# Kernel tuning notes

Hardware: AMD Instinct MI355X
Metric: run time of the kernel (lower is better)

Reference implementation:

```python
import jax, jax.numpy as jnp
import numpy as np


def _conv3x3(x, w):
    # x: [B,C,H,W], w: [O,I,3,3], SAME padding, no bias
    return jax.lax.conv_general_dilated(x, w, (1, 1), 'SAME',
                                        dimension_numbers=('NCHW', 'OIHW', 'NCHW'))


def _instance_norm(x, g, b, eps=1e-6):
    # normalize over spatial dims per (batch, channel)
    m = x.mean(axis=(2, 3), keepdims=True)
    v = x.var(axis=(2, 3), keepdims=True)
    xn = (x - m) * jax.lax.rsqrt(v + eps)
    return xn * g[None, :, None, None] + b[None, :, None, None]


def setup_inputs() -> dict:
    key = jax.random.key(0)
    ks = jax.random.split(key, 16)
    B, N, L = 1, 128, 256
    d_msa, d_pair, d_h = 256, 128, 32
    f32 = jnp.float32
    inp = {
        'msa': jax.random.normal(ks[0], (B, N, L, d_msa), f32),
        'pair': jax.random.normal(ks[1], (B, L, L, d_pair), f32),
        # LayerNorm(d_msa)
        'ln_g': jnp.ones((d_msa,), f32),
        'ln_b': jnp.zeros((d_msa,), f32),
        # proj_left / proj_right (lecun-normal-ish scale, zero bias)
        'Wl': jax.random.normal(ks[2], (d_msa, d_h), f32) * (1.0 / np.sqrt(d_msa)),
        'bl': jnp.zeros((d_h,), f32),
        'Wr': jax.random.normal(ks[3], (d_msa, d_h), f32) * (1.0 / np.sqrt(d_msa)),
        'br': jnp.zeros((d_h,), f32),
        # proj_out: (d_h*d_h) -> d_pair
        'Wo': jax.random.normal(ks[4], (d_h * d_h, d_pair), f32) * (1.0 / np.sqrt(d_h * d_h)),
        'bo': jnp.zeros((d_pair,), f32),
        # proj_down: (2*d_pair) -> d_pair, torch init eye_ -> identity block
        'Wd': jnp.concatenate([jnp.eye(d_pair, dtype=f32),
                               jnp.zeros((d_pair, d_pair), f32)], axis=0),
        'bd': jnp.zeros((d_pair,), f32),
        # ResBlock2D: two 3x3 convs (no bias) + affine InstanceNorm each
        'conv1': jax.random.normal(ks[5], (d_pair, d_pair, 3, 3), f32) * (1.0 / np.sqrt(9 * d_pair)),
        'in1_g': jnp.ones((d_pair,), f32),
        'in1_b': jnp.zeros((d_pair,), f32),
        'conv2': jax.random.normal(ks[6], (d_pair, d_pair, 3, 3), f32) * (1.0 / np.sqrt(9 * d_pair)),
        'in2_g': jnp.ones((d_pair,), f32),
        'in2_b': jnp.zeros((d_pair,), f32),
    }
    return inp


def reference(msa, pair, ln_g, ln_b, Wl, bl, Wr, br, Wo, bo, Wd, bd,
              conv1, in1_g, in1_b, conv2, in2_g, in2_b):
    B, N, L, _ = msa.shape
    # LayerNorm over d_msa (eps=1e-5, torch default)
    mu = msa.mean(-1, keepdims=True)
    var = msa.var(-1, keepdims=True)
    msa_n = (msa - mu) * jax.lax.rsqrt(var + 1e-5) * ln_g + ln_b
    left = msa_n @ Wl + bl                      # [B,N,L,h]
    right = (msa_n @ Wr + br) / float(N)        # [B,N,L,h]
    # MSA outer product over sequences: [B,L,L,h,h] -> [B,L,L,h*h]
    op = jnp.einsum('bsli,bsmj->blmij', left, right).reshape(B, L, L, -1)
    out = op @ Wo + bo                          # [B,L,L,d_pair]
    p = jnp.concatenate([pair, out], axis=-1) @ Wd + bd  # proj_down
    # ResidualNetwork(1 block): NCHW
    x = p.transpose(0, 3, 1, 2)
    h = _conv3x3(x, conv1)
    h = jax.nn.elu(_instance_norm(h, in1_g, in1_b))
    # dropout is identity at inference
    h = _conv3x3(h, conv2)
    h = _instance_norm(h, in2_g, in2_b)
    x = jax.nn.elu(x + h)
    return x.transpose(0, 2, 3, 1)              # [B,L,L,d_pair]
```

## Files before the change

### kernel.cpp

```cpp
#include <hip/hip_runtime.h>
#include <math.h>

#define LL 256
#define NS 128
#define DM 256
#define DH 32
#define DP 128
#define HW 65536

using u16 = unsigned short;
typedef __attribute__((ext_vector_type(8))) short s8v;
typedef __attribute__((ext_vector_type(4))) short s4v;
typedef __attribute__((ext_vector_type(4))) float f4v;

#define MFMA(a, b, c) __builtin_amdgcn_mfma_f32_16x16x32_bf16((a), (b), (c), 0, 0, 0)

__device__ __forceinline__ u16 f2bf(float f) {
  unsigned u = __float_as_uint(f);
  u = (u + 0x7FFFu + ((u >> 16) & 1u)) >> 16;
  return (u16)u;
}
__device__ __forceinline__ unsigned cvtpk2(float lo, float hi) {
  unsigned r;
  asm("v_cvt_pk_bf16_f32 %0, %1, %2" : "=v"(r) : "v"(lo), "v"(hi));
  return r;
}
__device__ __forceinline__ float bf2f(u16 h) { return __uint_as_float(((unsigned)h) << 16); }
__device__ __forceinline__ float elu1(float v) { return v > 0.f ? v : expm1f(v); }
__device__ __forceinline__ s8v zero8() {
  s8v v;
  #pragma unroll
  for (int j = 0; j < 8; ++j) v[j] = 0;
  return v;
}


__device__ __forceinline__ void prep_convw(const float* __restrict__ w,
                                           u16* __restrict__ wP, int idx)
{
  int h = idx & 3, co = (idx >> 2) & 127, kk = (idx >> 9) & 3, tap = idx >> 11;
  s8v o;
  #pragma unroll
  for (int j = 0; j < 8; ++j) {
    int ci = kk * 32 + h * 8 + j;
    o[j] = (short)f2bf(w[((size_t)co * DP + ci) * 9 + tap]);
  }
  *(s8v*)(wP + (size_t)idx * 8) = o;
}

__global__ __launch_bounds__(256) void k_prep_ln(
    const float* __restrict__ Wl, const float* __restrict__ Wr,
    const float* __restrict__ Wo, const float* __restrict__ Wd,
    const float* __restrict__ conv1, const float* __restrict__ conv2,
    const float* __restrict__ pair,
    const float* __restrict__ msa, const float* __restrict__ ln_g,
    const float* __restrict__ ln_b,
    u16* __restrict__ WlrF, u16* __restrict__ WoF, u16* __restrict__ WdF,
    u16* __restrict__ wP1, u16* __restrict__ wP2, u16* __restrict__ pairF,
    u16* __restrict__ msaF)
{
  __shared__ alignas(16) u16 buf[16 * 264];
  int bx = blockIdx.x, t = threadIdx.x;
  if (bx < 64) {
    int o = bx * 256 + t;
    int tile = o >> 6, u = o & 63;
    int cblk = tile >> 5, j = tile & 31;
    int kslot = u >> 4, cl = u & 15;
    int c = cblk * 16 + cl;
    s8v v;
    #pragma unroll
    for (int e = 0; e < 8; ++e) {
      int i = kslot * 8 + e;
      v[e] = (short)f2bf(Wo[(size_t)(i * 32 + j) * DP + c]);
    }
    *(s8v*)(WoF + (size_t)o * 8) = v;
  } else if (bx < 80) {
    int o = (bx - 64) * 256 + t;
    int tile = o >> 6, u = o & 63;
    int cblk = tile >> 3, kch = tile & 7;
    int kslot = u >> 4, cl = u & 15;
    int c = cblk * 16 + cl;
    s8v v;
    #pragma unroll
    for (int e = 0; e < 8; ++e) {
      int k = kch * 32 + kslot * 8 + e;
      v[e] = (short)f2bf(Wd[(size_t)k * DP + c]);
    }
    *(s8v*)(WdF + (size_t)o * 8) = v;
  } else if (bx < 88) {
    int o = (bx - 80) * 256 + t;
    int tile = o >> 6, u = o & 63;
    int nblk = tile >> 3, kch = tile & 7;
    int kslot = u >> 4, cl = u & 15;
    int n = nblk * 16 + cl;
    s8v v;
    #pragma unroll
    for (int e = 0; e < 8; ++e) {
      int k = kch * 32 + kslot * 8 + e;
      float x = (n < 32) ? Wl[k * DH + n] : Wr[k * DH + (n - 32)];
      v[e] = (short)f2bf(x);
    }
    *(s8v*)(WlrF + (size_t)o * 8) = v;
  } else if (bx < 160) {
    prep_convw(conv1, wP1, (bx - 88) * 256 + t);
  } else if (bx < 232) {
    prep_convw(conv2, wP2, (bx - 160) * 256 + t);
  } else if (bx < 4328) {
    int pb = bx - 232;
    #pragma unroll
    for (int it = 0; it < 2; ++it) {
      int idx = it * 256 + t;
      int pix = idx >> 5, f4i = idx & 31;
      float4 v = ((const float4*)pair)[(size_t)(pb * 16 + pix) * 32 + f4i];
      s4v o;
      o[0] = (short)f2bf(v.x); o[1] = (short)f2bf(v.y);
      o[2] = (short)f2bf(v.z); o[3] = (short)f2bf(v.w);
      *(s4v*)(buf + pix * 136 + f4i * 4) = o;
    }
    __syncthreads();
    int kch = t >> 6, u = t & 63;
    int kslot = u >> 4, cl = u & 15;
    int k0 = kch * 32 + kslot * 8;
    s8v v = *(const s8v*)(buf + cl * 136 + k0);
    *(s8v*)(pairF + ((size_t)pb * 256 + t) * 8) = v;
  } else {
    int bid = bx - 4328;
    int lane = t & 63, wid = t >> 6;
    int row0 = bid * 16;
    const float4 gv = ((const float4*)ln_g)[lane];
    const float4 bv = ((const float4*)ln_b)[lane];
    #pragma unroll
    for (int rr = 0; rr < 4; ++rr) {
      int row = row0 + wid * 4 + rr;
      float4 v = ((const float4*)(msa + (size_t)row * DM))[lane];
      float s = v.x + v.y + v.z + v.w;
      float q = v.x * v.x + v.y * v.y + v.z * v.z + v.w * v.w;
      #pragma unroll
      for (int off = 32; off; off >>= 1) { s += __shfl_down(s, off); q += __shfl_down(q, off); }
      s = __shfl(s, 0); q = __shfl(q, 0);
      float mean = s * (1.f / DM);
      float var  = q * (1.f / DM) - mean * mean;
      float rstd = rsqrtf(var + 1e-5f);
      s4v o;
      o[0] = (short)f2bf((v.x - mean) * rstd * gv.x + bv.x);
      o[1] = (short)f2bf((v.y - mean) * rstd * gv.y + bv.y);
      o[2] = (short)f2bf((v.z - mean) * rstd * gv.z + bv.z);
      o[3] = (short)f2bf((v.w - mean) * rstd * gv.w + bv.w);
      *(s4v*)(buf + (wid * 4 + rr) * 264 + lane * 4) = o;
    }
    __syncthreads();
    #pragma unroll
    for (int it = 0; it < 2; ++it) {
      int o = it * 256 + t;
      int kch = o >> 6, kslot = (o >> 4) & 3, rr = o & 15;
      int k0 = kch * 32 + kslot * 8;
      s8v v = *(const s8v*)(buf + rr * 264 + k0);
      *(s8v*)(msaF + (size_t)bid * 4096 + (size_t)o * 8) = v;
    }
  }
}

__global__ __launch_bounds__(256) void k_gemm_lr(const u16* __restrict__ msaF,
                                                 const u16* __restrict__ WlrF,
                                                 const float* __restrict__ bl,
                                                 const float* __restrict__ br,
                                                 u16* __restrict__ leftT,
                                                 u16* __restrict__ rightT)
{
  int lane = threadIdx.x & 63, wid = threadIdx.x >> 6;
  int sIdx = blockIdx.x;
  f4v acc[4][4] = {};
  #pragma unroll
  for (int ks = 0; ks < 8; ++ks) {
    s8v a[4], bb[4];
    #pragma unroll
    for (int mi = 0; mi < 4; ++mi)
      a[mi] = *(const s8v*)(msaF + ((size_t)(sIdx * 16 + wid * 4 + mi) * 8 + ks) * 512 + lane * 8);
    #pragma unroll
    for (int ni = 0; ni < 4; ++ni)
      bb[ni] = *(const s8v*)(WlrF + ((size_t)(ni * 8 + ks)) * 512 + lane * 8);
    #pragma unroll
    for (int mi = 0; mi < 4; ++mi)
      #pragma unroll
      for (int ni = 0; ni < 4; ++ni)
        acc[mi][ni] = MFMA(a[mi], bb[ni], acc[mi][ni]);
  }
  #pragma unroll
  for (int mi = 0; mi < 4; ++mi) {
    #pragma unroll
    for (int ni = 0; ni < 4; ++ni) {
      int n = ni * 16 + (lane & 15);
      #pragma unroll
      for (int r = 0; r < 4; ++r) {
        int l = wid * 64 + mi * 16 + (lane >> 4) * 4 + r;
        float v = acc[mi][ni][r];
        if (n < 32) {
          leftT[((size_t)l * 32 + n) * 128 + sIdx] = f2bf(v + bl[n]);
        } else {
          rightT[((size_t)l * 32 + (n - 32)) * 128 + sIdx] =
              f2bf((v + br[n - 32]) * (1.f / NS));
        }
      }
    }
  }
}

__global__ __launch_bounds__(256) void k_fragpack(const u16* __restrict__ leftT,
                                                  const u16* __restrict__ rightT,
                                                  u16* __restrict__ leftF,
                                                  u16* __restrict__ rightF)
{
  __shared__ alignas(16) u16 lds[64 * 136];
  int t = threadIdx.x, bx = blockIdx.x;
  bool isR = bx >= 128;
  int blk = isR ? (bx - 128) : bx;
  #pragma unroll
  for (int it = 0; it < 4; ++it) {
    int u = it * 256 + t;
    int row = u >> 4, sc = u & 15;
    const u16* src;
    if (!isR) {
      src = leftT + ((size_t)(blk * 64 + row)) * 128 + sc * 8;
    } else {
      int gcol = blk * 64 + row;
      int mg = gcol >> 10, rem = gcol & 1023;
      int jc = rem >> 8, nc = rem & 255;
      int m = mg * 32 + (nc >> 3), j = jc * 8 + (nc & 7);
      src = rightT + ((size_t)(m * 32 + j)) * 128 + sc * 8;
    }
    *(s8v*)(lds + row * 136 + sc * 8) = *(const s8v*)src;
  }
  __syncthreads();
  u16* dst = (isR ? rightF : leftF) + (size_t)blk * 8192;
  #pragma unroll
  for (int it = 0; it < 4; ++it) {
    int o = it * 256 + t;
    int tloc = o >> 6, u = o & 63;
    int rb = tloc >> 2, sc2 = tloc & 3;
    int kslot = u >> 4, rr = u & 15;
    int row = rb * 16 + rr, s0 = sc2 * 32 + kslot * 8;
    *(s8v*)(dst + (size_t)o * 8) = *(const s8v*)(lds + row * 136 + s0);
  }
}

__global__ __launch_bounds__(512, 4) void k_fused(
    const u16* __restrict__ leftF, const u16* __restrict__ rightF,
    const u16* __restrict__ WoF, const u16* __restrict__ pairF,
    const u16* __restrict__ WdF, const float* __restrict__ bo,
    const float* __restrict__ bd, u16* __restrict__ pN)
{
  __shared__ alignas(16) u16 Als[8192];
  __shared__ alignas(16) u16 opL[16384];
  __shared__ alignas(16) u16 obL[8192];
  int t = threadIdx.x, lane = t & 63, w = t >> 6;
  int rlo = lane & 15, slot = lane >> 4;
  int b = blockIdx.x;
  int mg = b & 7, lp = b >> 3;
  int l0 = lp * 2, m0 = mg * 32;

  #pragma unroll
  for (int i = 0; i < 2; ++i) {
    int u = t + 512 * i;
    *(s8v*)(Als + (size_t)u * 8) = *(const s8v*)(leftF + (size_t)lp * 8192 + (size_t)u * 8);
  }

  f4v acc2[4] = {};
  s8v bb[8];
  #pragma unroll
  for (int ks = 0; ks < 4; ++ks)
    #pragma unroll
    for (int ni = 0; ni < 2; ++ni)
      bb[ks * 2 + ni] = *(const s8v*)(rightF +
          ((size_t)((mg * 64 + 0 * 16 + w * 2 + ni) * 4 + ks)) * 512 + lane * 8);
  __syncthreads();

  #pragma unroll
  for (int jc = 0; jc < 4; ++jc) {
    f4v acc1[4][2] = {};
    __builtin_amdgcn_s_setprio(1);
    #pragma unroll
    for (int ks = 0; ks < 4; ++ks) {
      s8v a[4];
      #pragma unroll
      for (int mi = 0; mi < 4; ++mi)
        a[mi] = *(const s8v*)(Als + (size_t)(mi * 4 + ks) * 512 + lane * 8);
      #pragma unroll
      for (int mi = 0; mi < 4; ++mi)
        #pragma unroll
        for (int ni = 0; ni < 2; ++ni)
          acc1[mi][ni] = MFMA(a[mi], bb[ks * 2 + ni], acc1[mi][ni]);
    }
    __builtin_amdgcn_s_setprio(0);
    #pragma unroll
    for (int mi = 0; mi < 4; ++mi) {
      int i0 = (mi & 1) * 16 + slot * 4;
      int lLoc = mi >> 1;
      int kslot = (i0 >> 3) & 3;
      #pragma unroll
      for (int ni = 0; ni < 2; ++ni) {
        int n = w * 32 + ni * 16 + rlo;
        int pix = lLoc * 32 + (n >> 3);
        int jj = n & 7;
        uint2 o2;
        o2.x = cvtpk2(acc1[mi][ni][0], acc1[mi][ni][1]);
        o2.y = cvtpk2(acc1[mi][ni][2], acc1[mi][ni][3]);
        int byte = ((pix >> 4) * 8 + jj) * 1024 +
                   (kslot * 16 + ((pix & 15) ^ jj)) * 16 + (i0 & 7) * 2;
        *(uint2*)((char*)opL + byte) = o2;
      }
    }
    s8v wb[8];
    #pragma unroll
    for (int ks = 0; ks < 8; ++ks)
      wb[ks] = *(const s8v*)(WoF + ((size_t)(w * 32 + jc * 8 + ks)) * 512 + lane * 8);
    __syncthreads();
    __builtin_amdgcn_s_setprio(1);
    #pragma unroll
    for (int ks = 0; ks < 8; ++ks) {
      s8v a[4];
      #pragma unroll
      for (int mi = 0; mi < 4; ++mi) {
        int byte = (mi * 8 + ks) * 1024 + (slot * 16 + (rlo ^ ks)) * 16;
        a[mi] = *(const s8v*)((const char*)opL + byte);
      }
      #pragma unroll
      for (int mi = 0; mi < 4; ++mi)
        acc2[mi] = MFMA(a[mi], wb[ks], acc2[mi]);
    }
    __builtin_amdgcn_s_setprio(0);
    if (jc < 3) {
      #pragma unroll
      for (int ks = 0; ks < 4; ++ks)
        #pragma unroll
        for (int ni = 0; ni < 2; ++ni)
          bb[ks * 2 + ni] = *(const s8v*)(rightF +
              ((size_t)((mg * 64 + (jc + 1) * 16 + w * 2 + ni) * 4 + ks)) * 512 + lane * 8);
    }
    __syncthreads();
  }

  {
    int c = w * 16 + rlo;
    float bias = bo[c];
    #pragma unroll
    for (int mi = 0; mi < 4; ++mi)
      #pragma unroll
      for (int r = 0; r < 4; ++r) {
        int pix = mi * 16 + slot * 4 + r;
        int byte = (pix * 256 + c * 2) ^ ((pix & 7) << 4);
        *(u16*)((char*)obL + byte) = f2bf(acc2[mi][r] + bias);
      }
  }
  __syncthreads();

  int wr = w >> 2, wcq = w & 3;
  int pix0 = wr * 32, c0 = wcq * 32;
  {
    f4v acc[2][2] = {};
    #pragma unroll
    for (int ks = 0; ks < 4; ++ks) {
      s8v a[2], b2[2];
      #pragma unroll
      for (int mi = 0; mi < 2; ++mi) {
        int pb = (l0 + wr) * 16 + (m0 >> 4) + mi;
        a[mi] = *(const s8v*)(pairF + ((size_t)(pb * 4 + ks)) * 512 + lane * 8);
      }
      #pragma unroll
      for (int ni = 0; ni < 2; ++ni) {
        int cblk = wcq * 2 + ni;
        b2[ni] = *(const s8v*)(WdF + ((size_t)(cblk * 8 + ks)) * 512 + lane * 8);
      }
      #pragma unroll
      for (int mi = 0; mi < 2; ++mi)
        #pragma unroll
        for (int ni = 0; ni < 2; ++ni)
          acc[mi][ni] = MFMA(a[mi], b2[ni], acc[mi][ni]);
    }
    #pragma unroll
    for (int ks = 0; ks < 4; ++ks) {
      s8v a[2], b2[2];
      #pragma unroll
      for (int mi = 0; mi < 2; ++mi) {
        int pix = pix0 + mi * 16 + rlo;
        int k = ks * 32 + slot * 8;
        int byte = (pix * 256 + k * 2) ^ ((pix & 7) << 4);
        a[mi] = *(const s8v*)((const char*)obL + byte);
      }
      #pragma unroll
      for (int ni = 0; ni < 2; ++ni) {
        int cblk = wcq * 2 + ni;
        b2[ni] = *(const s8v*)(WdF + ((size_t)(cblk * 8 + 4 + ks)) * 512 + lane * 8);
      }
      #pragma unroll
      for (int mi = 0; mi < 2; ++mi)
        #pragma unroll
        for (int ni = 0; ni < 2; ++ni)
          acc[mi][ni] = MFMA(a[mi], b2[ni], acc[mi][ni]);
    }
    #pragma unroll
    for (int mi = 0; mi < 2; ++mi)
      #pragma unroll
      for (int ni = 0; ni < 2; ++ni) {
        int c = c0 + ni * 16 + rlo;
        float bias = bd[c];
        #pragma unroll
        for (int r = 0; r < 4; ++r) {
          int pix = pix0 + mi * 16 + slot * 4 + r;
          int byte = (pix * 256 + c * 2) ^ ((pix & 7) << 4);
          *(u16*)((char*)opL + byte) = f2bf(acc[mi][ni][r] + bias);
        }
      }
  }
  __syncthreads();

  #pragma unroll
  for (int q = 0; q < 2; ++q) {
    int u = q * 512 + t;
    int pix = u >> 4, off = u & 15;
    int byte = (pix * 256 + off * 16) ^ ((pix & 7) << 4);
    uint4 v = *(const uint4*)((const char*)opL + byte);
    int pixG = (l0 + (pix >> 5)) * 256 + m0 + (pix & 31);
    *(uint4*)(pN + (size_t)pixG * 128 + off * 8) = v;
  }
}

#define CLOADB(s, B) {                                                        \
    _Pragma("unroll")                                                         \
    for (int j = 0; j < 2; ++j) {                                             \
      const int st_ = (s) + j;                                                \
      _Pragma("unroll")                                                       \
      for (int ni = 0; ni < 4; ++ni) {                                        \
        int co_ = co0 + ni * 16 + rlo;                                        \
        B[j][ni] = *(const s8v*)(wP +                                         \
            ((size_t)(st_ * 128 + co_) * 4 + slot) * 8);                      \
      }                                                                       \
    } }
#define CSTEP2(s, B) {                                                        \
    _Pragma("unroll")                                                         \
    for (int j = 0; j < 2; ++j) {                                             \
      const int st_ = (s) + j, tap_ = st_ >> 2, kk_ = st_ & 3;                \
      const int dy_ = tap_ / 3, dx_ = tap_ % 3;                               \
      s8v a_[4];                                                              \
      _Pragma("unroll")                                                       \
      for (int mi = 0; mi < 4; ++mi) {                                        \
        int p_ = mi * 16 + rlo + dx_;                                         \
        int lb_ = (((wpy + dy_) * 66 + p_) * 256 + kk_ * 64 + slot * 16) ^    \
                  ((p_ & 7) << 4);                                            \
        a_[mi] = *(const s8v*)((const char*)Ast + lb_);                       \
      }                                                                       \
      __builtin_amdgcn_s_setprio(1);                                          \
      _Pragma("unroll")                                                       \
      for (int mi = 0; mi < 4; ++mi)                                          \
        _Pragma("unroll")                                                     \
        for (int ni = 0; ni < 4; ++ni)                                        \
          acc[mi][ni] = MFMA(a_[mi], B[j][ni], acc[mi][ni]);                  \
      __builtin_amdgcn_s_setprio(0);                                          \
    } }

template<bool FUSE_IN>
__global__ __launch_bounds__(256, 2) void k_conv(const u16* __restrict__ inN,
                                                 const float* __restrict__ gSin,
                                                 const float* __restrict__ gQin,
                                                 const float* __restrict__ ing,
                                                 const float* __restrict__ inb,
                                                 const u16* __restrict__ wP,
                                                 u16* __restrict__ outB,
                                                 float* __restrict__ gSout,
                                                 float* __restrict__ gQout)
{
  __shared__ alignas(16) u16 Ast[4 * 66 * 128];
  __shared__ float partS[4][64], partQ[4][64];
  __shared__ alignas(16) float sstat[256];
  __shared__ float red2[4][128];
  int t = threadIdx.x, lane = t & 63, w = t >> 6;
  int rlo = lane & 15, slot = lane >> 4;
  int b = blockIdx.x;
  int L = (b & 7) * 64 + (b >> 3);
  int xt = L & 3, yt = L >> 2;
  int x0 = xt * 64, y0 = yt * 2;

  if constexpr (FUSE_IN) {
    int c = t & 127, h = t >> 7;
    float s = 0.f, q = 0.f;
    for (int i = h * 256; i < h * 256 + 256; ++i) {
      s += gSin[i * 128 + c];
      q += gQin[i * 128 + c];
    }
    red2[h][c] = s; red2[2 + h][c] = q;
    __syncthreads();
    if (t < 128) {
      float ss = red2[0][t] + red2[1][t];
      float qq = red2[2][t] + red2[3][t];
      float m = ss * (1.f / HW);
      float var = qq * (1.f / HW) - m * m;
      float rstd = rsqrtf(var + 1e-6f);
      float sc = rstd * ing[t];
      sstat[t] = sc;
      sstat[128 + t] = inb[t] - m * sc;
    }
    __syncthreads();
  }

  for (int u = t; u < 4224; u += 256) {
    int r = u / 1056;
    int rem = u - r * 1056;
    int p = rem >> 4, ku = rem & 15;
    int gy = y0 + r - 1, gx = x0 - 1 + p;
    s8v v = zero8();
    if ((unsigned)gy < 256u && (unsigned)gx < 256u) {
      v = *(const s8v*)(inN + ((size_t)gy * LL + gx) * 128 + ku * 8);
      if constexpr (FUSE_IN) {
        float4 s0 = ((const float4*)sstat)[ku * 2];
        float4 s1 = ((const float4*)sstat)[ku * 2 + 1];
        float4 q0 = ((const float4*)(sstat + 128))[ku * 2];
        float4 q1 = ((const float4*)(sstat + 128))[ku * 2 + 1];
        float f0 = elu1(bf2f((u16)v[0]) * s0.x + q0.x);
        float f1 = elu1(bf2f((u16)v[1]) * s0.y + q0.y);
        float f2 = elu1(bf2f((u16)v[2]) * s0.z + q0.z);
        float f3 = elu1(bf2f((u16)v[3]) * s0.w + q0.w);
        float f4 = elu1(bf2f((u16)v[4]) * s1.x + q1.x);
        float f5 = elu1(bf2f((u16)v[5]) * s1.y + q1.y);
        float f6 = elu1(bf2f((u16)v[6]) * s1.z + q1.z);
        float f7 = elu1(bf2f((u16)v[7]) * s1.w + q1.w);
        uint4 uv;
        uv.x = cvtpk2(f0, f1); uv.y = cvtpk2(f2, f3);
        uv.z = cvtpk2(f4, f5); uv.w = cvtpk2(f6, f7);
        v = __builtin_bit_cast(s8v, uv);
      }
    }
    int lb = (u * 16) ^ ((p & 7) << 4);
    *(s8v*)((char*)Ast + lb) = v;
  }
  __syncthreads();
  int wpy = w >> 1, co0 = (w & 1) * 64;
  f4v acc[4][4] = {};
  s8v bA[2][4], bB[2][4];
  CLOADB(0, bA)
  #pragma unroll
  for (int s = 0; s < 36; s += 4) {
    CLOADB(s + 2, bB)
    CSTEP2(s, bA)
    if (s + 4 < 36) { CLOADB(s + 4, bA) }
    CSTEP2(s + 2, bB)
  }
  #pragma unroll
  for (int ni = 0; ni < 4; ++ni) {
    float s = 0.f, q = 0.f;
    #pragma unroll
    for (int mi = 0; mi < 4; ++mi)
      #pragma unroll
      for (int r = 0; r < 4; ++r) {
        float v = acc[mi][ni][r];
        s += v; q += v * v;
      }
    s += __shfl_xor(s, 16); s += __shfl_xor(s, 32);
    q += __shfl_xor(q, 16); q += __shfl_xor(q, 32);
    if (slot == 0) { partS[w][ni * 16 + rlo] = s; partQ[w][ni * 16 + rlo] = q; }
  }
  __syncthreads();
  float* AstF = (float*)Ast;
  #pragma unroll
  for (int mi = 0; mi < 4; ++mi)
    #pragma unroll
    for (int ni = 0; ni < 4; ++ni) {
      int co = co0 + ni * 16 + rlo;
      #pragma unroll
      for (int r = 0; r < 4; ++r) {
        int pix = mi * 16 + slot * 4 + r;
        int byte = wpy * 32768 + ((pix * 512 + co * 4) ^ ((pix & 7) << 4));
        *(float*)((char*)AstF + byte) = acc[mi][ni][r];
      }
    }
  if (t < 128) {
    int half = t >> 6, cl = t & 63;
    gSout[b * 128 + t] = partS[half][cl] + partS[2 + half][cl];
    gQout[b * 128 + t] = partQ[half][cl] + partQ[2 + half][cl];
  }
  __syncthreads();
  #pragma unroll
  for (int it = 0; it < 8; ++it) {
    int u = it * 256 + t;
    int wpy2 = u >> 10, rem = u & 1023;
    int pix = rem >> 4, cv8 = rem & 15;
    int base = wpy2 * 32768;
    int b0b = base + ((pix * 512 + cv8 * 32) ^ ((pix & 7) << 4));
    int b1b = base + ((pix * 512 + cv8 * 32 + 16) ^ ((pix & 7) << 4));
    float4 a = *(const float4*)((const char*)AstF + b0b);
    float4 bv = *(const float4*)((const char*)AstF + b1b);
    uint4 o;
    o.x = cvtpk2(a.x, a.y); o.y = cvtpk2(a.z, a.w);
    o.z = cvtpk2(bv.x, bv.y); o.w = cvtpk2(bv.z, bv.w);
    *(uint4*)(outB + ((size_t)(y0 + wpy2) * LL + x0 + pix) * 128 + cv8 * 8) = o;
  }
}

__global__ __launch_bounds__(512) void k_instat2(const float* __restrict__ gS,
                                                 const float* __restrict__ gQ,
                                                 const float* __restrict__ g,
                                                 const float* __restrict__ b,
                                                 float* __restrict__ st)
{
  __shared__ float redS[8], redQ[8];
  int c = blockIdx.x, t = threadIdx.x;
  int lane = t & 63, w = t >> 6;
  float s = gS[(size_t)t * 128 + c];
  float q = gQ[(size_t)t * 128 + c];
  #pragma unroll
  for (int off = 32; off; off >>= 1) {
    s += __shfl_down(s, off);
    q += __shfl_down(q, off);
  }
  if (lane == 0) { redS[w] = s; redQ[w] = q; }
  __syncthreads();
  if (t == 0) {
    float ss = 0.f, qq = 0.f;
    #pragma unroll
    for (int i = 0; i < 8; ++i) { ss += redS[i]; qq += redQ[i]; }
    float m = ss * (1.f / HW);
    float var = qq * (1.f / HW) - m * m;
    float rstd = rsqrtf(var + 1e-6f);
    float sc = rstd * g[c];
    st[c] = sc;
    st[128 + c] = b[c] - m * sc;
  }
}

__global__ __launch_bounds__(256) void k_final(const u16* __restrict__ pN,
                                               const u16* __restrict__ h2,
                                               const float* __restrict__ st,
                                               float* __restrict__ out)
{
  int i = blockIdx.x * 256 + threadIdx.x;
  int c8 = i & 15;
  uint4 hv = ((const uint4*)h2)[i];
  uint4 pv = ((const uint4*)pN)[i];
  float4 s0 = ((const float4*)st)[c8 * 2], s1 = ((const float4*)st)[c8 * 2 + 1];
  float4 q0 = ((const float4*)(st + 128))[c8 * 2], q1 = ((const float4*)(st + 128))[c8 * 2 + 1];
  float4 f0, f1;
  f0.x = bf2f((u16)(hv.x & 0xffff)) * s0.x + q0.x + bf2f((u16)(pv.x & 0xffff));
  f0.y = bf2f((u16)(hv.x >> 16))    * s0.y + q0.y + bf2f((u16)(pv.x >> 16));
  f0.z = bf2f((u16)(hv.y & 0xffff)) * s0.z + q0.z + bf2f((u16)(pv.y & 0xffff));
  f0.w = bf2f((u16)(hv.y >> 16))    * s0.w + q0.w + bf2f((u16)(pv.y >> 16));
  f1.x = bf2f((u16)(hv.z & 0xffff)) * s1.x + q1.x + bf2f((u16)(pv.z & 0xffff));
  f1.y = bf2f((u16)(hv.z >> 16))    * s1.y + q1.y + bf2f((u16)(pv.z >> 16));
  f1.z = bf2f((u16)(hv.w & 0xffff)) * s1.z + q1.z + bf2f((u16)(pv.w & 0xffff));
  f1.w = bf2f((u16)(hv.w >> 16))    * s1.w + q1.w + bf2f((u16)(pv.w >> 16));
  f0.x = elu1(f0.x); f0.y = elu1(f0.y); f0.z = elu1(f0.z); f0.w = elu1(f0.w);
  f1.x = elu1(f1.x); f1.y = elu1(f1.y); f1.z = elu1(f1.z); f1.w = elu1(f1.w);
  ((float4*)out)[(size_t)i * 2]     = f0;
  ((float4*)out)[(size_t)i * 2 + 1] = f1;
}

extern "C" void kernel_launch(void* const* d_in, const int* in_sizes, int n_in,
                              void* d_out, int out_size, void* d_ws, size_t ws_size,
                              hipStream_t stream)
{
  const float* msa   = (const float*)d_in[0];
  const float* pair  = (const float*)d_in[1];
  const float* ln_g  = (const float*)d_in[2];
  const float* ln_b  = (const float*)d_in[3];
  const float* Wl    = (const float*)d_in[4];
  const float* bl    = (const float*)d_in[5];
  const float* Wr    = (const float*)d_in[6];
  const float* br    = (const float*)d_in[7];
  const float* Wo    = (const float*)d_in[8];
  const float* bo    = (const float*)d_in[9];
  const float* Wd    = (const float*)d_in[10];
  const float* bd    = (const float*)d_in[11];
  const float* conv1 = (const float*)d_in[12];
  const float* in1_g = (const float*)d_in[13];
  const float* in1_b = (const float*)d_in[14];
  const float* conv2 = (const float*)d_in[15];
  const float* in2_g = (const float*)d_in[16];
  const float* in2_b = (const float*)d_in[17];
  float* out = (float*)d_out;

  float* ws = (float*)d_ws;
  const size_t F = 1048576;
  u16* msaF   = (u16*)ws;
  u16* leftT  = (u16*)(ws + 4 * F);
  u16* rightT = (u16*)(ws + 4 * F + F / 2);
  u16* leftF  = (u16*)(ws + 5 * F);
  u16* rightF = (u16*)(ws + 5 * F + F / 2);
  u16* pN     = (u16*)(ws + 6 * F);
  u16* h1raw  = (u16*)(ws + 10 * F);
  u16* h2raw  = (u16*)(ws + 14 * F);
  u16* pairF  = (u16*)(ws + 18 * F);
  float* gS1  = ws + 22 * F;
  float* gQ1  = ws + 22 * F + 65536;
  float* gS2  = ws + 22 * F + 131072;
  float* gQ2  = ws + 22 * F + 196608;
  float* stats = ws + 22 * F + 262144;
  u16* aux    = (u16*)(ws + 22 * F + 262400);
  u16* wP1    = aux;
  u16* wP2    = aux + 147456;
  u16* WoF    = aux + 294912;
  u16* WdF    = aux + 425984;
  u16* WlrF   = aux + 458752;

  k_prep_ln<<<dim3(6376), dim3(256), 0, stream>>>(Wl, Wr, Wo, Wd, conv1, conv2,
                                                  pair, msa, ln_g, ln_b,
                                                  WlrF, WoF, WdF, wP1, wP2, pairF, msaF);
  k_gemm_lr<<<dim3(128), dim3(256), 0, stream>>>(msaF, WlrF, bl, br, leftT, rightT);
  k_fragpack<<<dim3(256), dim3(256), 0, stream>>>(leftT, rightT, leftF, rightF);

  k_fused<<<dim3(1024), dim3(512), 0, stream>>>(leftF, rightF, WoF, pairF, WdF,
                                                bo, bd, pN);

  k_conv<false><<<dim3(512), dim3(256), 0, stream>>>(pN, nullptr, nullptr,
                                                     nullptr, nullptr,
                                                     wP1, h1raw, gS1, gQ1);
  k_conv<true><<<dim3(512), dim3(256), 0, stream>>>(h1raw, gS1, gQ1, in1_g, in1_b,
                                                    wP2, h2raw, gS2, gQ2);
  k_instat2<<<dim3(128), dim3(512), 0, stream>>>(gS2, gQ2, in2_g, in2_b, stats);

  k_final<<<dim3(4096), dim3(256), 0, stream>>>(pN, h2raw, stats, out);
}
```

Measured before the change: 179.7 us.

## Shrink conv tile to one output row per block, doubling grid size

The 3x3 conv kernel now computes a single output row of 64 pixels per block instead of two, with each wave covering 32 output channels across all 64 pixels rather than 64 channels across one row. LDS use drops to 3 halo rows and the launch bound rises to 3 blocks per CU, with twice as many blocks. The stats buffers and the reductions that read them are resized for 1024 partial sums. The aim is more occupancy and smaller per-wave accumulators, at the cost of more halo reloads (3 input rows per output row instead of 4 per 2) and more weight traffic per output.

```diff
diff --git a/kernel.cpp b/kernel.cpp
--- a/kernel.cpp
+++ b/kernel.cpp
@@ -429,7 +429,7 @@
     for (int j = 0; j < 2; ++j) {                                             \
       const int st_ = (s) + j;                                                \
       _Pragma("unroll")                                                       \
-      for (int ni = 0; ni < 4; ++ni) {                                        \
+      for (int ni = 0; ni < 2; ++ni) {                                        \
         int co_ = co0 + ni * 16 + rlo;                                        \
         B[j][ni] = *(const s8v*)(wP +                                         \
             ((size_t)(st_ * 128 + co_) * 4 + slot) * 8);                      \
@@ -444,7 +444,7 @@
       _Pragma("unroll")                                                       \
       for (int mi = 0; mi < 4; ++mi) {                                        \
         int p_ = mi * 16 + rlo + dx_;                                         \
-        int lb_ = (((wpy + dy_) * 66 + p_) * 256 + kk_ * 64 + slot * 16) ^    \
+        int lb_ = (((dy_) * 66 + p_) * 256 + kk_ * 64 + slot * 16) ^          \
                   ((p_ & 7) << 4);                                            \
         a_[mi] = *(const s8v*)((const char*)Ast + lb_);                       \
       }                                                                       \
@@ -452,13 +452,13 @@
       _Pragma("unroll")                                                       \
       for (int mi = 0; mi < 4; ++mi)                                          \
         _Pragma("unroll")                                                     \
-        for (int ni = 0; ni < 4; ++ni)                                        \
+        for (int ni = 0; ni < 2; ++ni)                                        \
           acc[mi][ni] = MFMA(a_[mi], B[j][ni], acc[mi][ni]);                  \
       __builtin_amdgcn_s_setprio(0);                                          \
     } }
 
 template<bool FUSE_IN>
-__global__ __launch_bounds__(256, 2) void k_conv(const u16* __restrict__ inN,
+__global__ __launch_bounds__(256, 3) void k_conv(const u16* __restrict__ inN,
                                                  const float* __restrict__ gSin,
                                                  const float* __restrict__ gQin,
                                                  const float* __restrict__ ing,
@@ -468,29 +468,30 @@
                                                  float* __restrict__ gSout,
                                                  float* __restrict__ gQout)
 {
-  __shared__ alignas(16) u16 Ast[4 * 66 * 128];
-  __shared__ float partS[4][64], partQ[4][64];
+  __shared__ alignas(16) u16 Ast[3 * 66 * 128];
   __shared__ alignas(16) float sstat[256];
-  __shared__ float red2[4][128];
   int t = threadIdx.x, lane = t & 63, w = t >> 6;
   int rlo = lane & 15, slot = lane >> 4;
   int b = blockIdx.x;
-  int L = (b & 7) * 64 + (b >> 3);
-  int xt = L & 3, yt = L >> 2;
-  int x0 = xt * 64, y0 = yt * 2;
+  int L = (b & 7) * 128 + (b >> 3);
+  int xt = L & 3, y0 = L >> 2;
+  int x0 = xt * 64;
+  float* partS = (float*)((char*)Ast + 32768);
+  float* partQ = partS + 128;
+  float* red2  = partQ + 128;
 
   if constexpr (FUSE_IN) {
     int c = t & 127, h = t >> 7;
     float s = 0.f, q = 0.f;
-    for (int i = h * 256; i < h * 256 + 256; ++i) {
-      s += gSin[i * 128 + c];
-      q += gQin[i * 128 + c];
-    }
-    red2[h][c] = s; red2[2 + h][c] = q;
+    for (int i = h * 512; i < h * 512 + 512; ++i) {
+      s += gSin[(size_t)i * 128 + c];
+      q += gQin[(size_t)i * 128 + c];
+    }
+    red2[h * 128 + c] = s; red2[256 + h * 128 + c] = q;
     __syncthreads();
     if (t < 128) {
-      float ss = red2[0][t] + red2[1][t];
-      float qq = red2[2][t] + red2[3][t];
+      float ss = red2[t] + red2[128 + t];
+      float qq = red2[256 + t] + red2[384 + t];
       float m = ss * (1.f / HW);
       float var = qq * (1.f / HW) - m * m;
       float rstd = rsqrtf(var + 1e-6f);
@@ -501,7 +502,7 @@
     __syncthreads();
   }
 
-  for (int u = t; u < 4224; u += 256) {
+  for (int u = t; u < 3168; u += 256) {
     int r = u / 1056;
     int rem = u - r * 1056;
     int p = rem >> 4, ku = rem & 15;
@@ -532,9 +533,9 @@
     *(s8v*)((char*)Ast + lb) = v;
   }
   __syncthreads();
-  int wpy = w >> 1, co0 = (w & 1) * 64;
-  f4v acc[4][4] = {};
-  s8v bA[2][4], bB[2][4];
+  int co0 = w * 32;
+  f4v acc[4][2] = {};
+  s8v bA[2][2], bB[2][2];
   CLOADB(0, bA)
   #pragma unroll
   for (int s = 0; s < 36; s += 4) {
@@ -543,8 +544,9 @@
     if (s + 4 < 36) { CLOADB(s + 4, bA) }
     CSTEP2(s + 2, bB)
   }
-  #pragma unroll
-  for (int ni = 0; ni < 4; ++ni) {
+  float sreg[2], qreg[2];
+  #pragma unroll
+  for (int ni = 0; ni < 2; ++ni) {
     float s = 0.f, q = 0.f;
     #pragma unroll
     for (int mi = 0; mi < 4; ++mi)
@@ -555,42 +557,46 @@
       }
     s += __shfl_xor(s, 16); s += __shfl_xor(s, 32);
     q += __shfl_xor(q, 16); q += __shfl_xor(q, 32);
-    if (slot == 0) { partS[w][ni * 16 + rlo] = s; partQ[w][ni * 16 + rlo] = q; }
+    sreg[ni] = s; qreg[ni] = q;
   }
   __syncthreads();
+  if (slot == 0) {
+    #pragma unroll
+    for (int ni = 0; ni < 2; ++ni) {
+      partS[co0 + ni * 16 + rlo] = sreg[ni];
+      partQ[co0 + ni * 16 + rlo] = qreg[ni];
+    }
+  }
   float* AstF = (float*)Ast;
   #pragma unroll
   for (int mi = 0; mi < 4; ++mi)
     #pragma unroll
-    for (int ni = 0; ni < 4; ++ni) {
+    for (int ni = 0; ni < 2; ++ni) {
       int co = co0 + ni * 16 + rlo;
       #pragma unroll
       for (int r = 0; r < 4; ++r) {
         int pix = mi * 16 + slot * 4 + r;
-        int byte = wpy * 32768 + ((pix * 512 + co * 4) ^ ((pix & 7) << 4));
+        int byte = (pix * 512 + co * 4) ^ ((pix & 7) << 4);
         *(float*)((char*)AstF + byte) = acc[mi][ni][r];
       }
     }
+  __syncthreads();
   if (t < 128) {
-    int half = t >> 6, cl = t & 63;
-    gSout[b * 128 + t] = partS[half][cl] + partS[2 + half][cl];
-    gQout[b * 128 + t] = partQ[half][cl] + partQ[2 + half][cl];
-  }
-  __syncthreads();
-  #pragma unroll
-  for (int it = 0; it < 8; ++it) {
+    gSout[(size_t)b * 128 + t] = partS[t];
+    gQout[(size_t)b * 128 + t] = partQ[t];
+  }
+  #pragma unroll
+  for (int it = 0; it < 4; ++it) {
     int u = it * 256 + t;
-    int wpy2 = u >> 10, rem = u & 1023;
-    int pix = rem >> 4, cv8 = rem & 15;
-    int base = wpy2 * 32768;
-    int b0b = base + ((pix * 512 + cv8 * 32) ^ ((pix & 7) << 4));
-    int b1b = base + ((pix * 512 + cv8 * 32 + 16) ^ ((pix & 7) << 4));
+    int pix = u >> 4, cv8 = u & 15;
+    int b0b = (pix * 512 + cv8 * 32) ^ ((pix & 7) << 4);
+    int b1b = (pix * 512 + cv8 * 32 + 16) ^ ((pix & 7) << 4);
     float4 a = *(const float4*)((const char*)AstF + b0b);
     float4 bv = *(const float4*)((const char*)AstF + b1b);
     uint4 o;
     o.x = cvtpk2(a.x, a.y); o.y = cvtpk2(a.z, a.w);
     o.z = cvtpk2(bv.x, bv.y); o.w = cvtpk2(bv.z, bv.w);
-    *(uint4*)(outB + ((size_t)(y0 + wpy2) * LL + x0 + pix) * 128 + cv8 * 8) = o;
+    *(uint4*)(outB + ((size_t)y0 * LL + x0 + pix) * 128 + cv8 * 8) = o;
   }
 }
 
@@ -603,8 +609,8 @@
   __shared__ float redS[8], redQ[8];
   int c = blockIdx.x, t = threadIdx.x;
   int lane = t & 63, w = t >> 6;
-  float s = gS[(size_t)t * 128 + c];
-  float q = gQ[(size_t)t * 128 + c];
+  float s = gS[(size_t)t * 128 + c] + gS[(size_t)(t + 512) * 128 + c];
+  float q = gQ[(size_t)t * 128 + c] + gQ[(size_t)(t + 512) * 128 + c];
   #pragma unroll
   for (int off = 32; off; off >>= 1) {
     s += __shfl_down(s, off);
@@ -687,11 +693,11 @@
   u16* h2raw  = (u16*)(ws + 14 * F);
   u16* pairF  = (u16*)(ws + 18 * F);
   float* gS1  = ws + 22 * F;
-  float* gQ1  = ws + 22 * F + 65536;
-  float* gS2  = ws + 22 * F + 131072;
-  float* gQ2  = ws + 22 * F + 196608;
-  float* stats = ws + 22 * F + 262144;
-  u16* aux    = (u16*)(ws + 22 * F + 262400);
+  float* gQ1  = ws + 22 * F + 131072;
+  float* gS2  = ws + 22 * F + 262144;
+  float* gQ2  = ws + 22 * F + 393216;
+  float* stats = ws + 22 * F + 524288;
+  u16* aux    = (u16*)(ws + 22 * F + 524544);
   u16* wP1    = aux;
   u16* wP2    = aux + 147456;
   u16* WoF    = aux + 294912;
@@ -707,11 +713,11 @@
   k_fused<<<dim3(1024), dim3(512), 0, stream>>>(leftF, rightF, WoF, pairF, WdF,
                                                 bo, bd, pN);
 
-  k_conv<false><<<dim3(512), dim3(256), 0, stream>>>(pN, nullptr, nullptr,
-                                                     nullptr, nullptr,
-                                                     wP1, h1raw, gS1, gQ1);
-  k_conv<true><<<dim3(512), dim3(256), 0, stream>>>(h1raw, gS1, gQ1, in1_g, in1_b,
-                                                    wP2, h2raw, gS2, gQ2);
+  k_conv<false><<<dim3(1024), dim3(256), 0, stream>>>(pN, nullptr, nullptr,
+                                                      nullptr, nullptr,
+                                                      wP1, h1raw, gS1, gQ1);
+  k_conv<true><<<dim3(1024), dim3(256), 0, stream>>>(h1raw, gS1, gQ1, in1_g, in1_b,
+                                                     wP2, h2raw, gS2, gQ2);
   k_instat2<<<dim3(128), dim3(512), 0, stream>>>(gS2, gQ2, in2_g, in2_b, stats);
 
   k_final<<<dim3(4096), dim3(256), 0, stream>>>(pN, h2raw, stats, out);
```

New measurement: 446.1 us. 2.48x slower.
